# Performance work log

Measured on AMD Instinct MI355X. Metric: run time of the kernel, lower is better.

Reference implementation:

```python
import jax, jax.numpy as jnp
import numpy as np

INPUT_SZ = 512
HIDDEN_SZ = 512
BATCH = 64
SEQ = 512


def setup_inputs() -> dict:
    key = jax.random.key(0)
    k_x, k_ih, k_hh = jax.random.split(key, 3)
    x = jax.random.normal(k_x, (BATCH, SEQ, INPUT_SZ), dtype=jnp.float32)
    # xavier-uniform style init for 2-D params, zeros for bias (as in init_weights)
    lim_ih = float(np.sqrt(6.0 / (INPUT_SZ + 4 * HIDDEN_SZ)))
    lim_hh = float(np.sqrt(6.0 / (HIDDEN_SZ + 4 * HIDDEN_SZ)))
    weight_ih = jax.random.uniform(k_ih, (INPUT_SZ, 4 * HIDDEN_SZ), jnp.float32, -lim_ih, lim_ih)
    weight_hh = jax.random.uniform(k_hh, (HIDDEN_SZ, 4 * HIDDEN_SZ), jnp.float32, -lim_hh, lim_hh)
    bias = jnp.zeros((4 * HIDDEN_SZ,), jnp.float32)
    h0 = jnp.zeros((1, BATCH, HIDDEN_SZ), jnp.float32)
    c0 = jnp.zeros((1, BATCH, HIDDEN_SZ), jnp.float32)
    return {"x": x, "weight_ih": weight_ih, "weight_hh": weight_hh, "bias": bias, "h0": h0, "c0": c0}


def reference(x, weight_ih, weight_hh, bias, h0, c0):
    HS = weight_hh.shape[0]
    # Precompute input projection for all timesteps: (seq, batch, 4*HS)
    x_proj = jnp.einsum('bsi,ih->sbh', x, weight_ih)

    def step(carry, xp_t):
        h_t, c_t = carry  # (1, b, HS)
        gates = xp_t[None] + h_t @ weight_hh + bias  # (1, b, 4*HS)
        i_t = jax.nn.sigmoid(gates[..., :HS])
        f_t = jax.nn.sigmoid(gates[..., HS:2 * HS])
        g_t = jnp.tanh(gates[..., 2 * HS:3 * HS])
        o_t = jax.nn.sigmoid(gates[..., 3 * HS:])
        c_t = f_t * c_t + i_t * g_t
        h_t = o_t * jnp.tanh(c_t)
        return (h_t, c_t), h_t[0]  # emit (b, HS)

    (h_T, c_T), hs = jax.lax.scan(step, (h0, c0), x_proj)
    hidden_seq = jnp.transpose(hs, (1, 0, 2))  # (batch, seq, HS)
    return hidden_seq, h_T, c_T
```

## Files before the change

kernel.cpp:

```cpp
#include <hip/hip_runtime.h>

#define SEQ   512
#define BATCH 64
#define IS    512
#define HS    512
#define G4    2048

typedef _Float16 half8 __attribute__((ext_vector_type(8)));
typedef _Float16 half4 __attribute__((ext_vector_type(4)));
typedef float floatx4 __attribute__((ext_vector_type(4)));
typedef unsigned long long ull;

__device__ __forceinline__ float sigm(float x) {
    return 1.0f / (1.0f + __expf(-x));
}
__device__ __forceinline__ float tanh_(float x) {
    float e = __expf(-2.0f * fabsf(x));
    float r = (1.0f - e) / (1.0f + e);
    return copysignf(r, x);
}

__global__ void convert_f32_f16(const float* __restrict__ in,
                                _Float16* __restrict__ out, int n4) {
    int i = blockIdx.x * blockDim.x + threadIdx.x;
    if (i < n4) {
        float4 v = ((const float4*)in)[i];
        half4 o = { (_Float16)v.x, (_Float16)v.y, (_Float16)v.z, (_Float16)v.w };
        ((half4*)out)[i] = o;
    }
}

__global__ void transpose_w(const float* __restrict__ in, _Float16* __restrict__ out) {
    __shared__ _Float16 tile[64][72];
    int bk = blockIdx.x & 7;
    int bn = blockIdx.x >> 3;
    int c = threadIdx.x & 63;
    int r4 = threadIdx.x >> 6;
    #pragma unroll
    for (int rr = 0; rr < 16; rr++) {
        int k = rr * 4 + r4;
        tile[k][c] = (_Float16)in[(size_t)(bk * 64 + k) * 2048 + bn * 64 + c];
    }
    __syncthreads();
    #pragma unroll
    for (int rr = 0; rr < 16; rr++) {
        int n = rr * 4 + r4;
        out[(size_t)(bn * 64 + n) * 512 + bk * 64 + c] = tile[c][n];
    }
}

__global__ void __launch_bounds__(256, 2) gemm_xproj(
    const _Float16* __restrict__ A,
    const _Float16* __restrict__ Bt,
    _Float16* __restrict__ xp) {
    __shared__ _Float16 As[4096];
    __shared__ _Float16 Bs[4096];
    const int tid = threadIdx.x;
    const int w = tid >> 6, l = tid & 63, lr = l & 15, q = l >> 4;
    const int bm = blockIdx.x & 255, bn = blockIdx.x >> 8;
    const int row0 = bm * 128, col0 = bn * 128;
    const int wr = (w >> 1) * 64, wc = (w & 1) * 64;

    floatx4 zz = {0.f, 0.f, 0.f, 0.f};
    floatx4 acc[4][4];
    #pragma unroll
    for (int mt = 0; mt < 4; mt++)
        #pragma unroll
        for (int ct = 0; ct < 4; ct++) acc[mt][ct] = zz;

    for (int kt = 0; kt < 16; kt++) {
        __syncthreads();
        #pragma unroll
        for (int rnd = 0; rnd < 2; rnd++) {
            int o = tid * 16 + rnd * 4096;
            int r = o >> 6;
            int ke = (o & 63) >> 1;
            *(half8*)((char*)As + o) = *(const half8*)(A  + (size_t)(row0 + r) * 512 + kt * 32 + ke);
            *(half8*)((char*)Bs + o) = *(const half8*)(Bt + (size_t)(col0 + r) * 512 + kt * 32 + ke);
        }
        __syncthreads();
        half8 af[4], bf[4];
        #pragma unroll
        for (int mt = 0; mt < 4; mt++)
            af[mt] = *(const half8*)(As + (wr + mt * 16 + lr) * 32 + q * 8);
        #pragma unroll
        for (int ct = 0; ct < 4; ct++)
            bf[ct] = *(const half8*)(Bs + (wc + ct * 16 + lr) * 32 + q * 8);
        #pragma unroll
        for (int mt = 0; mt < 4; mt++)
            #pragma unroll
            for (int ct = 0; ct < 4; ct++)
                acc[mt][ct] = __builtin_amdgcn_mfma_f32_16x16x32_f16(af[mt], bf[ct], acc[mt][ct], 0, 0, 0);
    }
    #pragma unroll
    for (int mt = 0; mt < 4; mt++) {
        #pragma unroll
        for (int r = 0; r < 4; r++) {
            int row = row0 + wr + mt * 16 + q * 4 + r;
            int t = row & 511, b = row >> 9;
            #pragma unroll
            for (int ct = 0; ct < 4; ct++) {
                int col = col0 + wc + ct * 16 + lr;
                int hid = col & 511, gate = col >> 9;
                int wgd = hid >> 4, u = hid & 15;
                xp[(size_t)(((t * 32 + wgd) * 64 + b)) * 64 + u * 4 + gate] =
                    (_Float16)acc[mt][ct][r];
            }
        }
    }
}

__global__ void __launch_bounds__(256, 1) lstm_scan(
    const _Float16* __restrict__ xp,
    const _Float16* __restrict__ wt,
    _Float16* __restrict__ hb,
    const float* __restrict__ bias,
    const float* __restrict__ h0,
    const float* __restrict__ c0,
    float* __restrict__ out,
    int* __restrict__ flags) {
    __shared__ _Float16 wlds[16384];
    __shared__ _Float16 scr[4 * 320];
    const int wg = blockIdx.x;
    const int tid = threadIdx.x;
    const int w = tid >> 6;
    const int l = tid & 63;
    const int lr = l & 15;
    const int q = l >> 4;
    const int myhid = wg * 16 + lr;
    _Float16* scrw = scr + w * 320;

    for (int idx = tid; idx < 2048; idx += 256) {
        int n = idx >> 6, g = idx & 63;
        int gate = n >> 4, u = n & 15;
        half8 v = *(const half8*)(wt + (size_t)(gate * 512 + wg * 16 + u) * 512 + g * 8);
        *(half8*)(wlds + n * 512 + ((g ^ (n & 7)) * 8)) = v;
    }
    half8 wreg[16][2];
    #pragma unroll
    for (int kt = 0; kt < 16; kt++)
        #pragma unroll
        for (int gg = 0; gg < 2; gg++)
            wreg[kt][gg] = *(const half8*)(wt + (size_t)((2 + gg) * 512 + wg * 16 + lr) * 512 + kt * 32 + q * 8);

    unsigned short* hbu = (unsigned short*)hb;
    for (int i = tid; i < 1024; i += 256) {
        int b = i >> 4, u = i & 15;
        union { _Float16 f; unsigned short us; } cv;
        cv.f = (_Float16)h0[b * 512 + wg * 16 + u];
        __hip_atomic_store(hbu + wg * 1024 + i, cv.us, __ATOMIC_RELAXED, __HIP_MEMORY_SCOPE_AGENT);
    }

    float bs[4], c[4];
    #pragma unroll
    for (int g4 = 0; g4 < 4; g4++) bs[g4] = bias[g4 * 512 + myhid];
    #pragma unroll
    for (int r = 0; r < 4; r++) c[r] = c0[(w * 16 + q * 4 + r) * 512 + myhid];

    asm volatile("s_waitcnt vmcnt(0)" ::: "memory");
    __syncthreads();
    if (tid == 0)
        __hip_atomic_store(&flags[wg * 32], 1, __ATOMIC_RELAXED, __HIP_MEMORY_SCOPE_AGENT);

    for (int t = 0; t < 512; t++) {
        float xpv[4][4];
        #pragma unroll
        for (int r = 0; r < 4; r++) {
            int b = w * 16 + q * 4 + r;
            half4 v = *(const half4*)(xp + (((size_t)t * 32 + wg) * 64 + b) * 64 + lr * 4);
            #pragma unroll
            for (int g4 = 0; g4 < 4; g4++) xpv[g4][r] = (float)v[g4];
        }

        if (tid < 32) {
            while (__hip_atomic_load(&flags[tid * 32], __ATOMIC_RELAXED,
                                     __HIP_MEMORY_SCOPE_AGENT) < t + 1)
                __builtin_amdgcn_s_sleep(1);
        }
        __syncthreads();

        const ull* hsrc = (const ull*)hb + (size_t)(t & 1) * 8192;
        const int b0 = w * 16 + lr;
        union HU { ull u[2]; half8 v; } a[16];
        #pragma unroll
        for (int kt = 0; kt < 16; kt++) {
            int idx = (2 * kt + (q >> 1)) * 256 + b0 * 4 + (q & 1) * 2;
            a[kt].u[0] = __hip_atomic_load(hsrc + idx,     __ATOMIC_RELAXED, __HIP_MEMORY_SCOPE_AGENT);
            a[kt].u[1] = __hip_atomic_load(hsrc + idx + 1, __ATOMIC_RELAXED, __HIP_MEMORY_SCOPE_AGENT);
        }

        floatx4 zz = {0.f, 0.f, 0.f, 0.f};
        floatx4 acc[4] = {zz, zz, zz, zz};
        #pragma unroll
        for (int kt = 0; kt < 16; kt++) {
            #pragma unroll
            for (int g4 = 0; g4 < 2; g4++) {
                int n = g4 * 16 + lr;
                half8 b8 = *(const half8*)(wlds + n * 512 + (((kt * 4 + q) ^ (n & 7)) * 8));
                acc[g4] = __builtin_amdgcn_mfma_f32_16x16x32_f16(a[kt].v, b8, acc[g4], 0, 0, 0);
            }
            #pragma unroll
            for (int gg = 0; gg < 2; gg++)
                acc[2 + gg] = __builtin_amdgcn_mfma_f32_16x16x32_f16(a[kt].v, wreg[kt][gg], acc[2 + gg], 0, 0, 0);
        }

        float hv[4];
        #pragma unroll
        for (int r = 0; r < 4; r++) {
            float gi = acc[0][r] + xpv[0][r] + bs[0];
            float gf = acc[1][r] + xpv[1][r] + bs[1];
            float gg = acc[2][r] + xpv[2][r] + bs[2];
            float go = acc[3][r] + xpv[3][r] + bs[3];
            float i_ = sigm(gi), f_ = sigm(gf), gv = tanh_(gg), o_ = sigm(go);
            c[r] = f_ * c[r] + i_ * gv;
            float h = o_ * tanh_(c[r]);
            hv[r] = h;
            scrw[(q * 4 + r) * 20 + lr] = (_Float16)h;
        }
        asm volatile("s_waitcnt lgkmcnt(0)" ::: "memory");
        union { half4 h; ull u; } pk;
        pk.h = *(const half4*)(scrw + (l >> 2) * 20 + (l & 3) * 4);
        ull* hdst = (ull*)hb + (size_t)((t + 1) & 1) * 8192 + wg * 256 + w * 64 + l;
        __hip_atomic_store(hdst, pk.u, __ATOMIC_RELAXED, __HIP_MEMORY_SCOPE_AGENT);

        asm volatile("s_waitcnt vmcnt(0)" ::: "memory");
        __syncthreads();
        if (tid == 0)
            __hip_atomic_store(&flags[wg * 32], t + 2, __ATOMIC_RELAXED, __HIP_MEMORY_SCOPE_AGENT);

        #pragma unroll
        for (int r = 0; r < 4; r++) {
            int b = w * 16 + q * 4 + r;
            out[(size_t)b * 262144 + (size_t)t * 512 + myhid] = hv[r];
            if (t == 511) {
                out[16777216 + b * 512 + myhid] = hv[r];
                out[16777216 + 32768 + b * 512 + myhid] = c[r];
            }
        }
    }
}

extern "C" void kernel_launch(void* const* d_in, const int* in_sizes, int n_in,
                              void* d_out, int out_size, void* d_ws, size_t ws_size,
                              hipStream_t stream) {
    const float* x    = (const float*)d_in[0];
    const float* wih  = (const float*)d_in[1];
    const float* whh  = (const float*)d_in[2];
    const float* bias = (const float*)d_in[3];
    const float* h0   = (const float*)d_in[4];
    const float* c0   = (const float*)d_in[5];
    float* out = (float*)d_out;

    char* ws = (char*)d_ws;
    _Float16* x16  = (_Float16*)(ws);
    _Float16* wtih = (_Float16*)(ws + 33554432);
    _Float16* wthh = (_Float16*)(ws + 35651584);
    _Float16* xp   = (_Float16*)(ws + 37748736);
    _Float16* hb   = (_Float16*)(ws + 171966464);
    int*      flags = (int*)(ws + 172097536);

    hipMemsetAsync(flags, 0, 4096, stream);
    convert_f32_f16<<<16384, 256, 0, stream>>>(x, x16, BATCH * SEQ * IS / 4);
    transpose_w<<<256, 256, 0, stream>>>(wih, wtih);
    transpose_w<<<256, 256, 0, stream>>>(whh, wthh);
    gemm_xproj<<<4096, 256, 0, stream>>>(x16, wtih, xp);
    lstm_scan<<<32, 256, 0, stream>>>(xp, wthh, hb, bias, h0, c0, out, flags);
}
```

Measured before the change: 2.392 ms.

## Replace flag barrier with poison-sentinel triple-buffered hidden state polling

Removes the per-step flag counters, spin-wait and block-wide barriers in the recurrent scan. Each step now writes h into one of three rotating buffers and poisons the next one, while readers spin until no loaded word equals the sentinel. The MFMA accumulation is also split into two independent chains to shorten dependency latency. The hidden buffer reuses workspace that the weight transposes occupied, and it is pre-filled with 0xFF. This relies on fp16 values never encoding as the all-ones pattern (NaN) and on no ordering problems between the poison and data stores.

```diff
diff --git a/kernel.cpp b/kernel.cpp
--- a/kernel.cpp
+++ b/kernel.cpp
@@ -117,8 +117,7 @@
     const float* __restrict__ bias,
     const float* __restrict__ h0,
     const float* __restrict__ c0,
-    float* __restrict__ out,
-    int* __restrict__ flags) {
+    float* __restrict__ out) {
     __shared__ _Float16 wlds[16384];
     __shared__ _Float16 scr[4 * 320];
     const int wg = blockIdx.x;
@@ -129,6 +128,7 @@
     const int q = l >> 4;
     const int myhid = wg * 16 + lr;
     _Float16* scrw = scr + w * 320;
+    const ull POISON = ~0ull;
 
     for (int idx = tid; idx < 2048; idx += 256) {
         int n = idx >> 6, g = idx & 63;
@@ -143,12 +143,14 @@
         for (int gg = 0; gg < 2; gg++)
             wreg[kt][gg] = *(const half8*)(wt + (size_t)((2 + gg) * 512 + wg * 16 + lr) * 512 + kt * 32 + q * 8);
 
-    unsigned short* hbu = (unsigned short*)hb;
-    for (int i = tid; i < 1024; i += 256) {
-        int b = i >> 4, u = i & 15;
-        union { _Float16 f; unsigned short us; } cv;
-        cv.f = (_Float16)h0[b * 512 + wg * 16 + u];
-        __hip_atomic_store(hbu + wg * 1024 + i, cv.us, __ATOMIC_RELAXED, __HIP_MEMORY_SCOPE_AGENT);
+    {
+        int b = tid >> 2, u4 = (tid & 3) * 4;
+        union { _Float16 h[4]; ull u; } pk;
+        #pragma unroll
+        for (int k2 = 0; k2 < 4; k2++)
+            pk.h[k2] = (_Float16)h0[b * 512 + wg * 16 + u4 + k2];
+        __hip_atomic_store((ull*)hb + wg * 256 + tid, pk.u,
+                           __ATOMIC_RELAXED, __HIP_MEMORY_SCOPE_AGENT);
     }
 
     float bs[4], c[4];
@@ -157,60 +159,65 @@
     #pragma unroll
     for (int r = 0; r < 4; r++) c[r] = c0[(w * 16 + q * 4 + r) * 512 + myhid];
 
-    asm volatile("s_waitcnt vmcnt(0)" ::: "memory");
     __syncthreads();
-    if (tid == 0)
-        __hip_atomic_store(&flags[wg * 32], 1, __ATOMIC_RELAXED, __HIP_MEMORY_SCOPE_AGENT);
-
+
+    int pr = 0, pw = 1, pp = 2;
     for (int t = 0; t < 512; t++) {
-        float xpv[4][4];
+        half4 xv[4];
         #pragma unroll
         for (int r = 0; r < 4; r++) {
             int b = w * 16 + q * 4 + r;
-            half4 v = *(const half4*)(xp + (((size_t)t * 32 + wg) * 64 + b) * 64 + lr * 4);
-            #pragma unroll
-            for (int g4 = 0; g4 < 4; g4++) xpv[g4][r] = (float)v[g4];
-        }
-
-        if (tid < 32) {
-            while (__hip_atomic_load(&flags[tid * 32], __ATOMIC_RELAXED,
-                                     __HIP_MEMORY_SCOPE_AGENT) < t + 1)
-                __builtin_amdgcn_s_sleep(1);
-        }
-        __syncthreads();
-
-        const ull* hsrc = (const ull*)hb + (size_t)(t & 1) * 8192;
+            xv[r] = *(const half4*)(xp + (((size_t)t * 32 + wg) * 64 + b) * 64 + lr * 4);
+        }
+
+        const ull* hsrc = (const ull*)hb + (size_t)pr * 8192;
         const int b0 = w * 16 + lr;
         union HU { ull u[2]; half8 v; } a[16];
-        #pragma unroll
-        for (int kt = 0; kt < 16; kt++) {
-            int idx = (2 * kt + (q >> 1)) * 256 + b0 * 4 + (q & 1) * 2;
-            a[kt].u[0] = __hip_atomic_load(hsrc + idx,     __ATOMIC_RELAXED, __HIP_MEMORY_SCOPE_AGENT);
-            a[kt].u[1] = __hip_atomic_load(hsrc + idx + 1, __ATOMIC_RELAXED, __HIP_MEMORY_SCOPE_AGENT);
-        }
+        int stale;
+        do {
+            stale = 0;
+            #pragma unroll
+            for (int kt = 0; kt < 16; kt++) {
+                int idx = (2 * kt + (q >> 1)) * 256 + b0 * 4 + (q & 1) * 2;
+                ull u0 = __hip_atomic_load(hsrc + idx,     __ATOMIC_RELAXED, __HIP_MEMORY_SCOPE_AGENT);
+                ull u1 = __hip_atomic_load(hsrc + idx + 1, __ATOMIC_RELAXED, __HIP_MEMORY_SCOPE_AGENT);
+                a[kt].u[0] = u0;
+                a[kt].u[1] = u1;
+                stale |= (int)(u0 == POISON) | (int)(u1 == POISON);
+            }
+        } while (stale);
 
         floatx4 zz = {0.f, 0.f, 0.f, 0.f};
         floatx4 acc[4] = {zz, zz, zz, zz};
+        floatx4 acc2[4] = {zz, zz, zz, zz};
         #pragma unroll
         for (int kt = 0; kt < 16; kt++) {
+            half8 bL[2];
             #pragma unroll
             for (int g4 = 0; g4 < 2; g4++) {
                 int n = g4 * 16 + lr;
-                half8 b8 = *(const half8*)(wlds + n * 512 + (((kt * 4 + q) ^ (n & 7)) * 8));
-                acc[g4] = __builtin_amdgcn_mfma_f32_16x16x32_f16(a[kt].v, b8, acc[g4], 0, 0, 0);
-            }
-            #pragma unroll
-            for (int gg = 0; gg < 2; gg++)
-                acc[2 + gg] = __builtin_amdgcn_mfma_f32_16x16x32_f16(a[kt].v, wreg[kt][gg], acc[2 + gg], 0, 0, 0);
+                bL[g4] = *(const half8*)(wlds + n * 512 + (((kt * 4 + q) ^ (n & 7)) * 8));
+            }
+            if ((kt & 1) == 0) {
+                acc[0] = __builtin_amdgcn_mfma_f32_16x16x32_f16(a[kt].v, bL[0], acc[0], 0, 0, 0);
+                acc[1] = __builtin_amdgcn_mfma_f32_16x16x32_f16(a[kt].v, bL[1], acc[1], 0, 0, 0);
+                acc[2] = __builtin_amdgcn_mfma_f32_16x16x32_f16(a[kt].v, wreg[kt][0], acc[2], 0, 0, 0);
+                acc[3] = __builtin_amdgcn_mfma_f32_16x16x32_f16(a[kt].v, wreg[kt][1], acc[3], 0, 0, 0);
+            } else {
+                acc2[0] = __builtin_amdgcn_mfma_f32_16x16x32_f16(a[kt].v, bL[0], acc2[0], 0, 0, 0);
+                acc2[1] = __builtin_amdgcn_mfma_f32_16x16x32_f16(a[kt].v, bL[1], acc2[1], 0, 0, 0);
+                acc2[2] = __builtin_amdgcn_mfma_f32_16x16x32_f16(a[kt].v, wreg[kt][0], acc2[2], 0, 0, 0);
+                acc2[3] = __builtin_amdgcn_mfma_f32_16x16x32_f16(a[kt].v, wreg[kt][1], acc2[3], 0, 0, 0);
+            }
         }
 
         float hv[4];
         #pragma unroll
         for (int r = 0; r < 4; r++) {
-            float gi = acc[0][r] + xpv[0][r] + bs[0];
-            float gf = acc[1][r] + xpv[1][r] + bs[1];
-            float gg = acc[2][r] + xpv[2][r] + bs[2];
-            float go = acc[3][r] + xpv[3][r] + bs[3];
+            float gi = acc[0][r] + acc2[0][r] + (float)xv[r][0] + bs[0];
+            float gf = acc[1][r] + acc2[1][r] + (float)xv[r][1] + bs[1];
+            float gg = acc[2][r] + acc2[2][r] + (float)xv[r][2] + bs[2];
+            float go = acc[3][r] + acc2[3][r] + (float)xv[r][3] + bs[3];
             float i_ = sigm(gi), f_ = sigm(gf), gv = tanh_(gg), o_ = sigm(go);
             c[r] = f_ * c[r] + i_ * gv;
             float h = o_ * tanh_(c[r]);
@@ -220,13 +227,13 @@
         asm volatile("s_waitcnt lgkmcnt(0)" ::: "memory");
         union { half4 h; ull u; } pk;
         pk.h = *(const half4*)(scrw + (l >> 2) * 20 + (l & 3) * 4);
-        ull* hdst = (ull*)hb + (size_t)((t + 1) & 1) * 8192 + wg * 256 + w * 64 + l;
-        __hip_atomic_store(hdst, pk.u, __ATOMIC_RELAXED, __HIP_MEMORY_SCOPE_AGENT);
 
         asm volatile("s_waitcnt vmcnt(0)" ::: "memory");
-        __syncthreads();
-        if (tid == 0)
-            __hip_atomic_store(&flags[wg * 32], t + 2, __ATOMIC_RELAXED, __HIP_MEMORY_SCOPE_AGENT);
+
+        __hip_atomic_store((ull*)hb + (size_t)pw * 8192 + wg * 256 + w * 64 + l, pk.u,
+                           __ATOMIC_RELAXED, __HIP_MEMORY_SCOPE_AGENT);
+        __hip_atomic_store((ull*)hb + (size_t)pp * 8192 + wg * 256 + w * 64 + l, POISON,
+                           __ATOMIC_RELAXED, __HIP_MEMORY_SCOPE_AGENT);
 
         #pragma unroll
         for (int r = 0; r < 4; r++) {
@@ -237,6 +244,8 @@
                 out[16777216 + 32768 + b * 512 + myhid] = c[r];
             }
         }
+
+        int tmp = pr; pr = pw; pw = pp; pp = tmp;
     }
 }
 
@@ -256,13 +265,12 @@
     _Float16* wtih = (_Float16*)(ws + 33554432);
     _Float16* wthh = (_Float16*)(ws + 35651584);
     _Float16* xp   = (_Float16*)(ws + 37748736);
-    _Float16* hb   = (_Float16*)(ws + 171966464);
-    int*      flags = (int*)(ws + 172097536);
-
-    hipMemsetAsync(flags, 0, 4096, stream);
+    _Float16* hb   = (_Float16*)(ws + 33554432);
+
     convert_f32_f16<<<16384, 256, 0, stream>>>(x, x16, BATCH * SEQ * IS / 4);
     transpose_w<<<256, 256, 0, stream>>>(wih, wtih);
     transpose_w<<<256, 256, 0, stream>>>(whh, wthh);
     gemm_xproj<<<4096, 256, 0, stream>>>(x16, wtih, xp);
-    lstm_scan<<<32, 256, 0, stream>>>(xp, wthh, hb, bias, h0, c0, out, flags);
-}
+    hipMemsetAsync(hb, 0xFF, 196608, stream);
+    lstm_scan<<<32, 256, 0, stream>>>(xp, wthh, hb, bias, h0, c0, out);
+}
```

New measurement: 2.331 ms. 1.03x faster.
